# Kernel tuning notes

Hardware: AMD Instinct MI355X
Metric: run time of the kernel (lower is better)

## Reference

```python
import jax, jax.numpy as jnp
import numpy as np

Q_HEADS, KV_HEADS, HEAD_DIM, WINDOW = 16, 4, 128, 512
HIDDEN = 2048
ROPE_BASE = 10000.0


def _rope_tables(T, head_dim, dtype):
    half = head_dim // 2
    inv_freq = 1.0 / (ROPE_BASE ** (jnp.arange(half, dtype=jnp.float32) / half))
    t = jnp.arange(T, dtype=jnp.float32)
    freqs = jnp.outer(t, inv_freq)  # [T, half]
    return jnp.cos(freqs).astype(dtype), jnp.sin(freqs).astype(dtype)


def _apply_rope(x, cos, sin):
    # x: [B, T, H, D]; cos/sin: [T, D//2] -> broadcast [1, T, 1, D//2]
    c = cos[None, :, None, :]
    s = sin[None, :, None, :]
    x1, x2 = jnp.split(x, 2, axis=-1)
    return jnp.concatenate([x1 * c - x2 * s, x1 * s + x2 * c], axis=-1)


def setup_inputs() -> dict:
    key = jax.random.key(0)
    ks = jax.random.split(key, 5)
    B, T = 1, 4096
    x = jax.random.normal(ks[0], (B, T, HIDDEN), dtype=jnp.float32)
    sc = 0.02
    wq = jax.random.normal(ks[1], (Q_HEADS * HEAD_DIM, HIDDEN), dtype=jnp.float32) * sc
    wk = jax.random.normal(ks[2], (KV_HEADS * HEAD_DIM, HIDDEN), dtype=jnp.float32) * sc
    wv = jax.random.normal(ks[3], (KV_HEADS * HEAD_DIM, HIDDEN), dtype=jnp.float32) * sc
    wo = jax.random.normal(ks[4], (HIDDEN, Q_HEADS * HEAD_DIM), dtype=jnp.float32) * sc
    return {"x": x, "wq": wq, "wk": wk, "wv": wv, "wo": wo}


def reference(x, wq, wk, wv, wo):
    B, T, _ = x.shape
    reps = Q_HEADS // KV_HEADS
    scale = 1.0 / np.sqrt(HEAD_DIM)

    q = jnp.einsum('bth,oh->bto', x, wq).reshape(B, T, Q_HEADS, HEAD_DIM)
    k = jnp.einsum('bth,oh->bto', x, wk).reshape(B, T, KV_HEADS, HEAD_DIM)
    v = jnp.einsum('bth,oh->bto', x, wv).reshape(B, T, KV_HEADS, HEAD_DIM)

    cos, sin = _rope_tables(T, HEAD_DIM, x.dtype)
    q = _apply_rope(q, cos, sin)
    k = _apply_rope(k, cos, sin)

    # GQA without materializing repeated K/V: group q as [B,T,KVH,reps,D]
    qg = q.reshape(B, T, KV_HEADS, reps, HEAD_DIM)
    scores = jnp.einsum('btgrd,bsgd->bgrts', qg, k) * scale  # [B,KVH,reps,T,T]

    idx = jnp.arange(T)
    # allowed: causal (s <= t) AND within window (t - s <= WINDOW)
    allowed = (idx[None, :] <= idx[:, None]) & (idx[:, None] - idx[None, :] <= WINDOW)
    scores = jnp.where(allowed[None, None, None], scores, jnp.finfo(scores.dtype).min)
    probs = jax.nn.softmax(scores, axis=-1)

    out = jnp.einsum('bgrts,bsgd->btgrd', probs, v)  # [B,T,KVH,reps,D]
    out = out.reshape(B, T, Q_HEADS * HEAD_DIM)
    return jnp.einsum('bto,ho->bth', out, wo)
```

## Files before the change

### kernel.cpp

```cpp
#include <hip/hip_runtime.h>

typedef __attribute__((ext_vector_type(8))) short short8;
typedef __attribute__((ext_vector_type(4))) float f32x4;
typedef __attribute__((ext_vector_type(4))) unsigned short u16x4;

__device__ __forceinline__ unsigned short f2b(float f) {
  unsigned int u = __float_as_uint(f);
  u += 0x7fffu + ((u >> 16) & 1u);
  return (unsigned short)(u >> 16);
}
__device__ __forceinline__ void glds16(const void* g, void* l) {
  __builtin_amdgcn_global_load_lds(
      (const __attribute__((address_space(1))) unsigned int*)g,
      (__attribute__((address_space(3))) unsigned int*)l, 16, 0, 0);
}

__global__ __launch_bounds__(256) void cast_all(const float* __restrict__ x,
                                                const float* __restrict__ wq,
                                                const float* __restrict__ wk,
                                                const float* __restrict__ wv,
                                                const float* __restrict__ wo,
                                                unsigned short* __restrict__ dst) {
  const int i = blockIdx.x * 256 + threadIdx.x;
  const float* s;
  int off;
  if (i < 2097152)      { s = x;  off = i; }
  else if (i < 3145728) { s = wq; off = i - 2097152; }
  else if (i < 3407872) { s = wk; off = i - 3145728; }
  else if (i < 3670016) { s = wv; off = i - 3407872; }
  else                  { s = wo; off = i - 3670016; }
  f32x4 v = ((const f32x4*)s)[off];
  u16x4 o;
  o[0] = f2b(v[0]); o[1] = f2b(v[1]); o[2] = f2b(v[2]); o[3] = f2b(v[3]);
  ((u16x4*)dst)[i] = o;
}

#define BARF()                            \
  asm volatile("" ::: "memory");          \
  __builtin_amdgcn_s_barrier();           \
  asm volatile("" ::: "memory");

__global__ __launch_bounds__(512, 4) void gemm_t128(
    const unsigned short* __restrict__ A, const unsigned short* __restrict__ B,
    const int mode,
    unsigned short* __restrict__ qb, unsigned short* __restrict__ kb,
    unsigned short* __restrict__ vtg, float* __restrict__ Cout) {
  extern __shared__ char smem[];
  const int tid = threadIdx.x;
  const int w = tid >> 6, lane = tid & 63;
  const int quad = lane >> 4, l15 = lane & 15;
  const int wm = w >> 2, wn = w & 3;
  const int m0 = blockIdx.x * 128;
  const int y  = blockIdx.y;
  const int n0 = y * 128;

  int cb[2];
  cb[0] = mode ? wn : wn * 2;
  cb[1] = mode ? wn + 4 : wn * 2 + 1;

  const int fragOff = l15 * 64 + ((quad * 16) ^ ((l15 & 8) << 2));
  const int sr = lane >> 2;
  const int sc = ((lane & 3) * 8) ^ ((lane & 32) ? 16 : 0);
  const unsigned short* const Abase = A + (size_t)(m0 + (w >> 1) * 16 + sr) * 2048 + (w & 1) * 32 + sc;
  const unsigned short* const Bbase = B + (size_t)(n0 + (w >> 1) * 16 + sr) * 2048 + (w & 1) * 32 + sc;

#define T_STAGE_A(tt)                                                                    \
  {                                                                                      \
    const int t_ = ((tt) < 32) ? (tt) : 31;                                              \
    char* const d_ = smem + (t_ & 1) * 32768 + w * 1024;                                 \
    glds16(Abase + (size_t)t_ * 64, d_);                                                 \
    glds16(Abase + (64 * 2048) + (size_t)t_ * 64, d_ + 8192);                            \
  }
#define T_STAGE_B(tt)                                                                    \
  {                                                                                      \
    const int t_ = ((tt) < 32) ? (tt) : 31;                                              \
    char* const d_ = smem + (t_ & 1) * 32768 + 16384 + w * 1024;                         \
    glds16(Bbase + (size_t)t_ * 64, d_);                                                 \
    glds16(Bbase + (64 * 2048) + (size_t)t_ * 64, d_ + 8192);                            \
  }
#define T_RD_AHI(c)                                                                      \
  _Pragma("unroll") for (int mi = 2; mi < 4; ++mi)                                       \
  _Pragma("unroll") for (int kk = 0; kk < 2; ++kk)                                       \
      af[mi][kk] = *(const short8*)(smem + (c) * 32768 + ((wm * 4 + mi) * 2 + kk) * 1024 + fragOff);
#define T_RD_ALO(c)                                                                      \
  _Pragma("unroll") for (int mi = 0; mi < 2; ++mi)                                       \
  _Pragma("unroll") for (int kk = 0; kk < 2; ++kk)                                       \
      af[mi][kk] = *(const short8*)(smem + (c) * 32768 + ((wm * 4 + mi) * 2 + kk) * 1024 + fragOff);
#define T_RD_B(c)                                                                        \
  _Pragma("unroll") for (int ni = 0; ni < 2; ++ni)                                       \
  _Pragma("unroll") for (int kk = 0; kk < 2; ++kk)                                       \
      bf[ni][kk] = *(const short8*)(smem + (c) * 32768 + 16384 + (cb[ni] * 2 + kk) * 1024 + fragOff);

  f32x4 acc[4][2];
  const f32x4 fz = {0.f, 0.f, 0.f, 0.f};
#pragma unroll
  for (int i = 0; i < 4; ++i) { acc[i][0] = fz; acc[i][1] = fz; }

  short8 af[4][2], bf[2][2];

#define T_MFMA(MI0)                                                              \
  _Pragma("unroll") for (int kk = 0; kk < 2; ++kk)                               \
  _Pragma("unroll") for (int mi = 0; mi < 2; ++mi)                               \
  _Pragma("unroll") for (int ni = 0; ni < 2; ++ni)                               \
      acc[(MI0) + mi][ni] = __builtin_amdgcn_mfma_f32_16x16x32_bf16(             \
          af[(MI0) + mi][kk], bf[ni][kk], acc[(MI0) + mi][ni], 0, 0, 0);

  T_STAGE_A(0) T_STAGE_B(0) T_STAGE_A(1)
  asm volatile("s_waitcnt vmcnt(2)" ::: "memory");
  BARF()

#define T_TILE(c, tt)                                                                \
   T_RD_AHI(c)                                                               \
  asm volatile("" ::: "memory");                                                     \
  T_RD_ALO(c) T_RD_B(c)                                                              \
  T_STAGE_B((tt) + 1)                                                                \
  BARF()                                                                             \
  __builtin_amdgcn_s_setprio(1); T_MFMA(0) __builtin_amdgcn_s_setprio(0);            \
  BARF()                                                                             \
   T_STAGE_A((tt) + 2)                                                       \
  BARF()                                                                             \
  __builtin_amdgcn_s_setprio(1); T_MFMA(2) __builtin_amdgcn_s_setprio(0);            \
  asm volatile("s_waitcnt vmcnt(2)" ::: "memory");                                   \
  BARF()

#pragma unroll 1
  for (int T = 0; T < 32; T += 2) {
    T_TILE(0, T)
    T_TILE(1, T + 1)
  }
  asm volatile("s_waitcnt vmcnt(0)" ::: "memory");
#undef T_TILE
#undef T_MFMA
#undef T_RD_AHI
#undef T_RD_ALO
#undef T_RD_B
#undef T_STAGE_A
#undef T_STAGE_B

  const int tb0 = m0 + wm * 64;
  if (mode == 0) {
#pragma unroll
    for (int mi = 0; mi < 4; ++mi) {
      const int row = tb0 + mi * 16 + quad * 4;
#pragma unroll
      for (int ni = 0; ni < 2; ++ni) {
        const int col = n0 + cb[ni] * 16 + l15;
#pragma unroll
        for (int r = 0; r < 4; ++r)
          Cout[(size_t)(row + r) * 2048 + col] = acc[mi][ni][r];
      }
    }
    return;
  }
  if (y >= 20) {
    const int g = y - 20;
#pragma unroll
    for (int mi = 0; mi < 4; ++mi) {
      const int tb = tb0 + mi * 16 + quad * 4;
#pragma unroll
      for (int ni = 0; ni < 2; ++ni) {
        const int d = cb[ni] * 16 + l15;
        u16x4 o;
#pragma unroll
        for (int r = 0; r < 4; ++r) o[r] = f2b(acc[mi][ni][r]);
        *(u16x4*)(vtg + (size_t)(g * 128 + d) * 4096 + tb) = o;
      }
    }
  } else {
    unsigned short* dst;
    int stride, hoff;
    if (y < 16) { dst = qb; stride = 2048; hoff = y * 128; }
    else        { dst = kb; stride = 512;  hoff = (y - 16) * 128; }
    const float c2 = 0.20762050593045889f;
    const float inv2pi = 0.15915494309189535f;
    const int i = wn * 16 + l15;
    const float inv_rev = exp2f(-(float)i * c2) * inv2pi;
#pragma unroll
    for (int mi = 0; mi < 4; ++mi) {
#pragma unroll
      for (int r = 0; r < 4; ++r) {
        const int t = tb0 + mi * 16 + quad * 4 + r;
        float rev = (float)t * inv_rev;
        rev -= floorf(rev);
        const float sn = __builtin_amdgcn_sinf(rev);
        const float cs = __builtin_amdgcn_cosf(rev);
        const float x1 = acc[mi][0][r], x2 = acc[mi][1][r];
        unsigned short* p = dst + (size_t)t * stride + hoff + i;
        p[0]  = f2b(x1 * cs - x2 * sn);
        p[64] = f2b(x1 * sn + x2 * cs);
      }
    }
  }
}

__global__ __launch_bounds__(256) void attn_fwd(const unsigned short* __restrict__ qp,
                                                const unsigned short* __restrict__ kp,
                                                const unsigned short* __restrict__ vtg,
                                                unsigned short* __restrict__ op) {
  __shared__ unsigned short Ks[2][4][1024];
  __shared__ unsigned short Vt[2][4096];
  const int tid = threadIdx.x;
  const int w = tid >> 6, lane = tid & 63;
  const int quad = lane >> 4, l15 = lane & 15;
  const int t0 = blockIdx.x * 32;
  const int g = blockIdx.y;
  const int h = g * 4 + w;
  const f32x4 fzero = {0.f, 0.f, 0.f, 0.f};
  const float scale = 0.088388347648318447f;
  const float NEG_INF = -__builtin_inff();

  short8 qf[4][2];
#pragma unroll
  for (int qt = 0; qt < 2; qt++) {
    const unsigned short* qrow = qp + (size_t)(t0 + qt * 16 + l15) * 2048 + h * 128 + quad * 8;
#pragma unroll
    for (int kb = 0; kb < 4; kb++) qf[kb][qt] = *(const short8*)(qrow + kb * 32);
  }

  f32x4 oacc[8][2];
#pragma unroll
  for (int db = 0; db < 8; db++) { oacc[db][0] = fzero; oacc[db][1] = fzero; }
  float Mrow[2] = {-1.0e30f, -1.0e30f}, Lrow[2] = {0.f, 0.f};

  const int s_begin = (t0 >= 512) ? (t0 - 512) : 0;
  const int nch = ((t0 + 31 - s_begin) >> 5) + 1;

  const int r4 = lane >> 2, c4 = lane & 3;
#define ATTN_STAGE(s0_, b_)                                                              \
  {                                                                                      \
    const int s0v = (s0_);                                                               \
    _Pragma("unroll")                                                                    \
    for (int p = 0; p < 2; p++)                                                          \
      glds16(kp + (size_t)(s0v + p * 16 + r4) * 512 + g * 128 + w * 32 + c4 * 8,         \
             &Ks[b_][w][p * 512]);                                                       \
    _Pragma("unroll")                                                                    \
    for (int p = 0; p < 2; p++)                                                          \
      glds16(vtg + (size_t)(g * 128 + w * 32 + p * 16 + r4) * 4096 + s0v + c4 * 8,       \
             &Vt[b_][w * 1024 + p * 512]);                                               \
  }

  ATTN_STAGE(s_begin, 0);

  for (int c = 0; c < nch; ++c) {
    const int s0 = s_begin + c * 32;
    const int b = c & 1;
    __syncthreads();
    if (c + 1 < nch) ATTN_STAGE(s_begin + (c + 1) * 32, (c + 1) & 1);

    {
      f32x4 sacc[2][2];
      sacc[0][0] = fzero; sacc[0][1] = fzero; sacc[1][0] = fzero; sacc[1][1] = fzero;
      const int permBase = ((l15 >> 2) << 3) + (l15 & 3);
#pragma unroll
      for (int kb = 0; kb < 4; kb++) {
        short8 af0 = *(const short8*)&Ks[b][kb][(permBase + 0) * 32 + quad * 8];
        short8 af1 = *(const short8*)&Ks[b][kb][(permBase + 4) * 32 + quad * 8];
        sacc[0][0] = __builtin_amdgcn_mfma_f32_16x16x32_bf16(af0, qf[kb][0], sacc[0][0], 0, 0, 0);
        sacc[0][1] = __builtin_amdgcn_mfma_f32_16x16x32_bf16(af0, qf[kb][1], sacc[0][1], 0, 0, 0);
        sacc[1][0] = __builtin_amdgcn_mfma_f32_16x16x32_bf16(af1, qf[kb][0], sacc[1][0], 0, 0, 0);
        sacc[1][1] = __builtin_amdgcn_mfma_f32_16x16x32_bf16(af1, qf[kb][1], sacc[1][1], 0, 0, 0);
      }

      short8 pb[2];
      float alpha[2];
#pragma unroll
      for (int qt = 0; qt < 2; qt++) {
        const int tq = t0 + qt * 16 + l15;
        float vals[8];
        float cmax = NEG_INF;
#pragma unroll
        for (int kt = 0; kt < 2; kt++)
#pragma unroll
          for (int r = 0; r < 4; r++) {
            const int s = s0 + quad * 8 + kt * 4 + r;
            const bool ok = (unsigned)(tq - s) <= 512u;
            const float v = ok ? sacc[kt][qt][r] * scale : NEG_INF;
            vals[kt * 4 + r] = v;
            cmax = fmaxf(cmax, v);
          }
        cmax = fmaxf(cmax, __shfl_xor(cmax, 16));
        cmax = fmaxf(cmax, __shfl_xor(cmax, 32));
        const float Mnew = fmaxf(Mrow[qt], cmax);
        alpha[qt] = __expf(Mrow[qt] - Mnew);
        Mrow[qt] = Mnew;
        float csum = 0.f;
#pragma unroll
        for (int j = 0; j < 8; j++) {
          const float p = __expf(vals[j] - Mnew);
          csum += p;
          pb[qt][j] = (short)f2b(p);
        }
        csum += __shfl_xor(csum, 16);
        csum += __shfl_xor(csum, 32);
        Lrow[qt] = Lrow[qt] * alpha[qt] + csum;
      }

#pragma unroll
      for (int db = 0; db < 8; db++) {
        short8 vf = *(const short8*)&Vt[b][(db * 16 + l15) * 32 + quad * 8];
#pragma unroll
        for (int qt = 0; qt < 2; qt++) {
          oacc[db][qt][0] *= alpha[qt]; oacc[db][qt][1] *= alpha[qt];
          oacc[db][qt][2] *= alpha[qt]; oacc[db][qt][3] *= alpha[qt];
          oacc[db][qt] = __builtin_amdgcn_mfma_f32_16x16x32_bf16(vf, pb[qt], oacc[db][qt], 0, 0, 0);
        }
      }
    }
  }
#undef ATTN_STAGE

#pragma unroll
  for (int qt = 0; qt < 2; qt++) {
    const float invL = 1.f / Lrow[qt];
    unsigned short* orow = op + (size_t)(t0 + qt * 16 + l15) * 2048 + h * 128;
#pragma unroll
    for (int db = 0; db < 8; db++) {
      u16x4 o;
#pragma unroll
      for (int r = 0; r < 4; r++) o[r] = f2b(oacc[db][qt][r] * invL);
      *(u16x4*)(orow + db * 16 + quad * 4) = o;
    }
  }
}

extern "C" void kernel_launch(void* const* d_in, const int* in_sizes, int n_in,
                              void* d_out, int out_size, void* d_ws, size_t ws_size,
                              hipStream_t stream) {
  const float* x  = (const float*)d_in[0];
  const float* wq = (const float*)d_in[1];
  const float* wk = (const float*)d_in[2];
  const float* wv = (const float*)d_in[3];
  const float* wo = (const float*)d_in[4];
  float* out = (float*)d_out;
  char* ws = (char*)d_ws;

  unsigned short* xb    = (unsigned short*)(ws + 0);
  unsigned short* wqkv  = (unsigned short*)(ws + 16777216);
  unsigned short* wob   = (unsigned short*)(ws + 29360128);
  unsigned short* qb    = (unsigned short*)(ws + 37748736);
  unsigned short* kbuf  = (unsigned short*)(ws + 54525952);
  unsigned short* vtg   = (unsigned short*)(ws + 58720256);
  unsigned short* attnb = xb;

  static bool attr_done = false;
  if (!attr_done) {
    hipFuncSetAttribute(reinterpret_cast<const void*>(gemm_t128),
                        hipFuncAttributeMaxDynamicSharedMemorySize, 65536);
    attr_done = true;
  }

  cast_all<<<18432, 256, 0, stream>>>(x, wq, wk, wv, wo, (unsigned short*)ws);

  gemm_t128<<<dim3(32, 24), 512, 65536, stream>>>(xb, wqkv, 1, qb, kbuf, vtg, nullptr);

  attn_fwd<<<dim3(128, 4), 256, 0, stream>>>(qb, kbuf, vtg, attnb);

  gemm_t128<<<dim3(32, 16), 512, 65536, stream>>>(attnb, wob, 0,
                                                  nullptr, nullptr, nullptr, out);
}
```

Baseline: 255.3 us.

## Widen attention blocks to 64 queries with split K/V loaders and swizzled LDS

The attention kernel now runs 512-thread blocks covering 64 query rows, with two groups of four waves sharing each staged K/V chunk. This halves how often each K/V tile is fetched. Loading is split so waves 0-3 fetch K and waves 4-7 fetch V, and XOR swizzles on the LDS columns are meant to cut bank conflicts on the fragment reads. Waves skip chunks that fall outside their own window, but the chunk loop is longer and the block count halves, which lowers parallelism across the GPU.

```diff
diff --git a/kernel.cpp b/kernel.cpp
--- a/kernel.cpp
+++ b/kernel.cpp
@@ -193,7 +193,7 @@
   }
 }
 
-__global__ __launch_bounds__(256) void attn_fwd(const unsigned short* __restrict__ qp,
+__global__ __launch_bounds__(512) void attn_fwd(const unsigned short* __restrict__ qp,
                                                 const unsigned short* __restrict__ kp,
                                                 const unsigned short* __restrict__ vtg,
                                                 unsigned short* __restrict__ op) {
@@ -202,9 +202,10 @@
   const int tid = threadIdx.x;
   const int w = tid >> 6, lane = tid & 63;
   const int quad = lane >> 4, l15 = lane & 15;
-  const int t0 = blockIdx.x * 32;
+  const int t0 = blockIdx.x * 64;
   const int g = blockIdx.y;
-  const int h = g * 4 + w;
+  const int h = g * 4 + (w & 3);
+  const int t0w = t0 + (w >> 2) * 32;
   const f32x4 fzero = {0.f, 0.f, 0.f, 0.f};
   const float scale = 0.088388347648318447f;
   const float NEG_INF = -__builtin_inff();
@@ -212,7 +213,7 @@
   short8 qf[4][2];
 #pragma unroll
   for (int qt = 0; qt < 2; qt++) {
-    const unsigned short* qrow = qp + (size_t)(t0 + qt * 16 + l15) * 2048 + h * 128 + quad * 8;
+    const unsigned short* qrow = qp + (size_t)(t0w + qt * 16 + l15) * 2048 + h * 128 + quad * 8;
 #pragma unroll
     for (int kb = 0; kb < 4; kb++) qf[kb][qt] = *(const short8*)(qrow + kb * 32);
   }
@@ -223,20 +224,28 @@
   float Mrow[2] = {-1.0e30f, -1.0e30f}, Lrow[2] = {0.f, 0.f};
 
   const int s_begin = (t0 >= 512) ? (t0 - 512) : 0;
-  const int nch = ((t0 + 31 - s_begin) >> 5) + 1;
+  const int nch = ((t0 + 63 - s_begin) >> 5) + 1;
 
   const int r4 = lane >> 2, c4 = lane & 3;
 #define ATTN_STAGE(s0_, b_)                                                              \
   {                                                                                      \
     const int s0v = (s0_);                                                               \
-    _Pragma("unroll")                                                                    \
-    for (int p = 0; p < 2; p++)                                                          \
-      glds16(kp + (size_t)(s0v + p * 16 + r4) * 512 + g * 128 + w * 32 + c4 * 8,         \
-             &Ks[b_][w][p * 512]);                                                       \
-    _Pragma("unroll")                                                                    \
-    for (int p = 0; p < 2; p++)                                                          \
-      glds16(vtg + (size_t)(g * 128 + w * 32 + p * 16 + r4) * 4096 + s0v + c4 * 8,       \
-             &Vt[b_][w * 1024 + p * 512]);                                               \
+    if (w < 4) {                                                                         \
+      _Pragma("unroll")                                                                  \
+      for (int p = 0; p < 2; p++) {                                                      \
+        const int kkey = p * 16 + r4;                                                    \
+        const int hk = ((kkey >> 1) ^ (kkey >> 3)) & 3;                                  \
+        glds16(kp + (size_t)(s0v + kkey) * 512 + g * 128 + w * 32 + (c4 ^ hk) * 8,       \
+               &Ks[b_][w][p * 512]);                                                     \
+      }                                                                                  \
+    } else {                                                                             \
+      const int wv = w - 4;                                                              \
+      const int hv = (r4 >> 1) & 3;                                                      \
+      _Pragma("unroll")                                                                  \
+      for (int p = 0; p < 2; p++)                                                        \
+        glds16(vtg + (size_t)(g * 128 + wv * 32 + p * 16 + r4) * 4096 + s0v + (c4 ^ hv) * 8, \
+               &Vt[b_][wv * 1024 + p * 512]);                                            \
+    }                                                                                    \
   }
 
   ATTN_STAGE(s_begin, 0);
@@ -247,14 +256,17 @@
     __syncthreads();
     if (c + 1 < nch) ATTN_STAGE(s_begin + (c + 1) * 32, (c + 1) & 1);
 
-    {
+    if (s0 + 31 >= t0w - 512 && s0 <= t0w + 31) {
       f32x4 sacc[2][2];
       sacc[0][0] = fzero; sacc[0][1] = fzero; sacc[1][0] = fzero; sacc[1][1] = fzero;
       const int permBase = ((l15 >> 2) << 3) + (l15 & 3);
+      const int row0 = permBase, row1 = permBase + 4;
+      const int co0 = ((quad ^ (((row0 >> 1) ^ (row0 >> 3)) & 3)) * 8);
+      const int co1 = ((quad ^ (((row1 >> 1) ^ (row1 >> 3)) & 3)) * 8);
 #pragma unroll
       for (int kb = 0; kb < 4; kb++) {
-        short8 af0 = *(const short8*)&Ks[b][kb][(permBase + 0) * 32 + quad * 8];
-        short8 af1 = *(const short8*)&Ks[b][kb][(permBase + 4) * 32 + quad * 8];
+        short8 af0 = *(const short8*)&Ks[b][kb][row0 * 32 + co0];
+        short8 af1 = *(const short8*)&Ks[b][kb][row1 * 32 + co1];
         sacc[0][0] = __builtin_amdgcn_mfma_f32_16x16x32_bf16(af0, qf[kb][0], sacc[0][0], 0, 0, 0);
         sacc[0][1] = __builtin_amdgcn_mfma_f32_16x16x32_bf16(af0, qf[kb][1], sacc[0][1], 0, 0, 0);
         sacc[1][0] = __builtin_amdgcn_mfma_f32_16x16x32_bf16(af1, qf[kb][0], sacc[1][0], 0, 0, 0);
@@ -265,7 +277,7 @@
       float alpha[2];
 #pragma unroll
       for (int qt = 0; qt < 2; qt++) {
-        const int tq = t0 + qt * 16 + l15;
+        const int tq = t0w + qt * 16 + l15;
         float vals[8];
         float cmax = NEG_INF;
 #pragma unroll
@@ -295,9 +307,10 @@
         Lrow[qt] = Lrow[qt] * alpha[qt] + csum;
       }
 
+      const int vco = (quad ^ ((l15 >> 1) & 3)) * 8;
 #pragma unroll
       for (int db = 0; db < 8; db++) {
-        short8 vf = *(const short8*)&Vt[b][(db * 16 + l15) * 32 + quad * 8];
+        short8 vf = *(const short8*)&Vt[b][(db * 16 + l15) * 32 + vco];
 #pragma unroll
         for (int qt = 0; qt < 2; qt++) {
           oacc[db][qt][0] *= alpha[qt]; oacc[db][qt][1] *= alpha[qt];
@@ -312,7 +325,7 @@
 #pragma unroll
   for (int qt = 0; qt < 2; qt++) {
     const float invL = 1.f / Lrow[qt];
-    unsigned short* orow = op + (size_t)(t0 + qt * 16 + l15) * 2048 + h * 128;
+    unsigned short* orow = op + (size_t)(t0w + qt * 16 + l15) * 2048 + h * 128;
 #pragma unroll
     for (int db = 0; db < 8; db++) {
       u16x4 o;
@@ -353,7 +366,7 @@
 
   gemm_t128<<<dim3(32, 24), 512, 65536, stream>>>(xb, wqkv, 1, qb, kbuf, vtg, nullptr);
 
-  attn_fwd<<<dim3(128, 4), 256, 0, stream>>>(qb, kbuf, vtg, attnb);
+  attn_fwd<<<dim3(64, 4), 512, 0, stream>>>(qb, kbuf, vtg, attnb);
 
   gemm_t128<<<dim3(32, 16), 512, 65536, stream>>>(attnb, wob, 0,
                                                   nullptr, nullptr, nullptr, out);
```

Result: faster. 240.3 us (-5.9%).
